# Performance work log

Measured on AMD Instinct MI355X. Metric: run time of the kernel, lower is better.

## Reference

```python
import jax, jax.numpy as jnp
import numpy as np

N_NODES = 50000
N_EDGES = 800000
N_NF = 16
N_EF = 8
HID = 300
MSG = 128
N_HIDDEN = 300
N_PRED = 8
N_GRAPHS = 64


def _lin_init(key, fan_in, fan_out):
    kw, kb = jax.random.split(key)
    lim = 1.0 / np.sqrt(fan_in)
    w = jax.random.uniform(kw, (fan_in, fan_out), minval=-lim, maxval=lim, dtype=jnp.float32)
    b = jax.random.uniform(kb, (fan_out,), minval=-lim, maxval=lim, dtype=jnp.float32)
    return w, b


def setup_inputs() -> dict:
    key = jax.random.key(0)
    ks = jax.random.split(key, 16)
    x = jax.random.normal(ks[0], (N_NODES, N_NF), dtype=jnp.float32)
    edge_index = jax.random.randint(ks[1], (2, N_EDGES), 0, N_NODES, dtype=jnp.int32)
    edge_attr = jax.random.normal(ks[2], (N_EDGES, N_EF), dtype=jnp.float32)
    batch = jnp.sort(jax.random.randint(ks[3], (N_NODES,), 0, N_GRAPHS, dtype=jnp.int32))
    # message MLP: (2*n_nf+n_ef) -> 300 -> 300 -> 300 -> msg_dim
    mw1, mb1 = _lin_init(ks[4], 2 * N_NF + N_EF, HID)
    mw2, mb2 = _lin_init(ks[5], HID, HID)
    mw3, mb3 = _lin_init(ks[6], HID, HID)
    mw4, mb4 = _lin_init(ks[7], HID, MSG)
    # node MLP: msg_dim -> 300 -> 300 -> 300 -> n_hidden
    nw1, nb1 = _lin_init(ks[8], MSG, HID)
    nw2, nb2 = _lin_init(ks[9], HID, HID)
    nw3, nb3 = _lin_init(ks[10], HID, HID)
    nw4, nb4 = _lin_init(ks[11], HID, N_HIDDEN)
    # final linear: n_hidden -> n_predict
    lw, lb = _lin_init(ks[12], N_HIDDEN, N_PRED)
    return {
        "x": x, "edge_index": edge_index, "edge_attr": edge_attr, "batch": batch,
        "mw1": mw1, "mb1": mb1, "mw2": mw2, "mb2": mb2, "mw3": mw3, "mb3": mb3,
        "mw4": mw4, "mb4": mb4,
        "nw1": nw1, "nb1": nb1, "nw2": nw2, "nb2": nb2, "nw3": nw3, "nb3": nb3,
        "nw4": nw4, "nb4": nb4, "lw": lw, "lb": lb,
    }


def reference(x, edge_index, edge_attr, batch,
              mw1, mb1, mw2, mb2, mw3, mb3, mw4, mb4,
              nw1, nb1, nw2, nb2, nw3, nb3, nw4, nb4, lw, lb):
    src = edge_index[0]  # x_j (source, PyG flow source_to_target)
    dst = edge_index[1]  # x_i (target), also scatter destination
    # message: cat([x_i, x_j, e_ij]) -> MLP
    tmp = jnp.concatenate([x[dst], x[src], edge_attr], axis=1)  # [E, 2*n_nf+n_ef]
    h = jax.nn.relu(tmp @ mw1 + mb1)
    h = jax.nn.relu(h @ mw2 + mb2)
    h = jax.nn.relu(h @ mw3 + mb3)
    msg = h @ mw4 + mb4  # [E, msg_dim]
    # aggregate: scatter-add into target nodes
    aggr = jax.ops.segment_sum(msg, dst, num_segments=N_NODES)  # [N, msg_dim]
    # update: node MLP
    h = jax.nn.relu(aggr @ nw1 + nb1)
    h = jax.nn.relu(h @ nw2 + nb2)
    h = jax.nn.relu(h @ nw3 + nb3)
    node = h @ nw4 + nb4  # [N, n_hidden]
    # global mean pool over graphs
    sums = jax.ops.segment_sum(node, batch, num_segments=N_GRAPHS)
    counts = jax.ops.segment_sum(jnp.ones((node.shape[0],), node.dtype), batch, num_segments=N_GRAPHS)
    pooled = sums / jnp.maximum(counts, 1.0)[:, None]  # [G, n_hidden]
    # dropout(p=0.5, training=self.training) is identity in eval mode
    return pooled @ lw + lb  # [G, n_predict]
```

## Files before the change

### kernel.cpp

```cpp
#include <hip/hip_runtime.h>
#include <hip/hip_bf16.h>
#include <stdint.h>

#define E_TOTAL 800000
#define NNODES  50000
#define NGRAPHS 64
#define NPRED   8
#define MPAD    50048
#define EBLK    6250
#define NBLK    391

#define TILE_B  40960
#define SCR_B   81920
#define LDSZ    (2*TILE_B + SCR_B)

typedef short v8s __attribute__((ext_vector_type(8)));
typedef float v4f __attribute__((ext_vector_type(4)));
typedef float f4  __attribute__((ext_vector_type(4)));

__device__ __forceinline__ void gload_lds16(const void* g, void* l) {
    __builtin_amdgcn_global_load_lds(
        (const __attribute__((address_space(1))) uint32_t*)g,
        (__attribute__((address_space(3))) uint32_t*)l, 16, 0, 0);
}

__device__ __forceinline__ short f2bf_s(float f) {
    __hip_bfloat16 h = __float2bfloat16(f);
    return *reinterpret_cast<short*>(&h);
}

template <bool EDGE>
__global__ __launch_bounds__(512)
void chain_kernel(const float* __restrict__ x, const int* __restrict__ ei,
                  const float* __restrict__ ea,
                  const __hip_bfloat16* __restrict__ aggrb,
                  const char* __restrict__ wimg,
                  const float* __restrict__ b1, const float* __restrict__ b2,
                  const float* __restrict__ b3, const float* __restrict__ b4,
                  float* __restrict__ outp)
{
    __shared__ __align__(16) char lds[LDSZ];
    const int tid  = threadIdx.x;
    const int lane = tid & 63;
    const int wave = tid >> 6;
    const int wr   = wave >> 2;
    const int wc   = wave & 3;
    const int l15  = lane & 15;
    const int kk   = lane >> 4;
    char* scr = lds + 2*TILE_B;
    const int rowbase = blockIdx.x*128 + wr*64;

    constexpr int KT1 = EDGE ? 1 : 2;
    constexpr int T   = KT1 + 15;

    auto stagef = [&](int t, int slot_){
        const char* s = wimg + (size_t)t*TILE_B + (size_t)tid*16;
        char* d = lds + slot_*TILE_B + wave*1024;
#pragma unroll
        for (int i = 0; i < 5; ++i) gload_lds16(s + i*8192, d + i*8192);
    };

    v4f acc[4][5];
#pragma unroll
    for (int p = 0; p < 4; ++p)
#pragma unroll
        for (int n = 0; n < 5; ++n) acc[p][n] = (v4f){0.f,0.f,0.f,0.f};

    float bb1[5], bb2[5], bb3[5], bb4[5];
#pragma unroll
    for (int n = 0; n < 5; ++n) {
        int colb = wc*80 + n*16 + l15;
        bb1[n] = b1[colb]; bb2[n] = b2[colb]; bb3[n] = b3[colb];
        if (EDGE) bb4[n] = (n < 2) ? b4[wc*32 + n*16 + l15] : 0.f;
        else      bb4[n] = b4[colb];
    }

    v8s af1[KT1][4][2];
    if (EDGE) {
#pragma unroll
        for (int p = 0; p < 4; ++p) {
            const int e = rowbase + p*16 + l15;
            const int nidx = (kk < 2) ? ei[E_TOTAL + e] : ei[e];
            const float* xs = x + (size_t)nidx*16 + (kk & 1)*8;
            f4 p0 = *(const f4*)xs, p1 = *(const f4*)(xs + 4);
            v8s a0, a1;
#pragma unroll
            for (int j = 0; j < 4; ++j) { a0[j] = f2bf_s(p0[j]); a0[4+j] = f2bf_s(p1[j]); }
            if (kk == 0) {
                const float* es = ea + (size_t)e*8;
                f4 q0 = *(const f4*)es, q1 = *(const f4*)(es + 4);
#pragma unroll
                for (int j = 0; j < 4; ++j) { a1[j] = f2bf_s(q0[j]); a1[4+j] = f2bf_s(q1[j]); }
            } else {
#pragma unroll
                for (int j = 0; j < 8; ++j) a1[j] = 0;
            }
            af1[0][p][0] = a0; af1[0][p][1] = a1;
        }
    } else {
#pragma unroll
        for (int p = 0; p < 4; ++p) {
            const int grow = rowbase + p*16 + l15;
#pragma unroll
            for (int t2 = 0; t2 < KT1; ++t2)
#pragma unroll
                for (int h = 0; h < 2; ++h)
                    af1[t2][p][h] = *(const v8s*)((const char*)aggrb +
                        (size_t)grow*256 + t2*128 + h*64 + kk*16);
        }
    }

    stagef(0, 0);
    int tt = 0, slot = 0;

#define TILE_BEGIN()                                                            \
    { asm volatile("s_waitcnt vmcnt(0)" ::: "memory");                          \
      __builtin_amdgcn_s_barrier();                                             \
      if (tt + 1 < T) stagef(tt + 1, slot ^ 1); }

#define TILE_END()  { ++tt; slot ^= 1; }

#define MFMA_TILE(A_, NT_, CB_)                                                 \
    { const char* sl_ = lds + slot*TILE_B;                                      \
      _Pragma("unroll")                                                         \
      for (int h_ = 0; h_ < 2; ++h_) {                                          \
        _Pragma("unroll")                                                       \
        for (int n_ = 0; n_ < NT_; ++n_) {                                      \
          int r_ = (CB_) + n_*16 + l15;                                         \
          v8s b_ = *(const v8s*)(sl_ + r_*128 + ((((h_<<2)|kk) ^ (r_&7))<<4));  \
          _Pragma("unroll")                                                     \
          for (int p_ = 0; p_ < 4; ++p_)                                        \
            acc[p_][n_] = __builtin_amdgcn_mfma_f32_16x16x32_bf16(              \
                (A_)[p_][h_], b_, acc[p_][n_], 0, 0, 0);                        \
        } } }

#define LOAD_AFRAG(KT_, A_)                                                     \
    { _Pragma("unroll")                                                         \
      for (int p_ = 0; p_ < 4; ++p_)                                            \
        _Pragma("unroll")                                                       \
        for (int h_ = 0; h_ < 2; ++h_) {                                        \
          int c_ = ((KT_)*8 + h_*4 + kk) ^ (l15 & 7);                           \
          (A_)[p_][h_] = *(const v8s*)(scr + (wr*64 + p_*16 + l15)*640 + (c_<<4)); \
        } }

#define DUMP_RELU(BB_)                                                          \
    { __builtin_amdgcn_s_barrier();        \
      _Pragma("unroll")                                                         \
      for (int p_ = 0; p_ < 4; ++p_)                                            \
        _Pragma("unroll")                                                       \
        for (int n_ = 0; n_ < 5; ++n_) {                                        \
          int col_ = wc*80 + n_*16 + l15;                                       \
          _Pragma("unroll")                                                     \
          for (int rr_ = 0; rr_ < 4; ++rr_) {                                   \
            int row_ = wr*64 + p_*16 + kk*4 + rr_;                              \
            float v_ = fmaxf(acc[p_][n_][rr_] + (BB_)[n_], 0.f);                \
            *(__hip_bfloat16*)(scr + row_*640 +                                 \
                (((col_>>3) ^ (row_&7))<<4) + (col_&7)*2) = __float2bfloat16(v_); \
          }                                                                     \
          acc[p_][n_] = (v4f){0.f,0.f,0.f,0.f};                                 \
        }                                                                       \
      asm volatile("s_waitcnt lgkmcnt(0)" ::: "memory"); }

#pragma unroll
    for (int kt = 0; kt < KT1; ++kt) { TILE_BEGIN(); MFMA_TILE(af1[kt], 5, wc*80); TILE_END(); }
    DUMP_RELU(bb1);
#pragma unroll
    for (int kt = 0; kt < 5; ++kt) {
        TILE_BEGIN(); v8s A_[4][2]; LOAD_AFRAG(kt, A_); MFMA_TILE(A_, 5, wc*80); TILE_END();
    }
    DUMP_RELU(bb2);
#pragma unroll
    for (int kt = 0; kt < 5; ++kt) {
        TILE_BEGIN(); v8s A_[4][2]; LOAD_AFRAG(kt, A_); MFMA_TILE(A_, 5, wc*80); TILE_END();
    }
    DUMP_RELU(bb3);
    if (EDGE) {
#pragma unroll
        for (int kt = 0; kt < 5; ++kt) {
            TILE_BEGIN(); v8s A_[4][2]; LOAD_AFRAG(kt, A_); MFMA_TILE(A_, 2, wc*32); TILE_END();
        }
#pragma unroll
        for (int p = 0; p < 4; ++p) {
#pragma unroll
            for (int rr = 0; rr < 4; ++rr) {
                int erow = rowbase + p*16 + kk*4 + rr;
                int d = ei[E_TOTAL + erow];
                float* ag = outp + (size_t)d*128;
#pragma unroll
                for (int n = 0; n < 2; ++n) {
                    int col = wc*32 + n*16 + l15;
                    atomicAdd(ag + col, acc[p][n][rr] + bb4[n]);
                }
            }
        }
    } else {
#pragma unroll
        for (int kt = 0; kt < 5; ++kt) {
            TILE_BEGIN(); v8s A_[4][2]; LOAD_AFRAG(kt, A_); MFMA_TILE(A_, 5, wc*80); TILE_END();
        }
#pragma unroll
        for (int p = 0; p < 4; ++p) {
#pragma unroll
            for (int n = 0; n < 5; ++n) {
                int col = wc*80 + n*16 + l15;
#pragma unroll
                for (int rr = 0; rr < 4; ++rr) {
                    int grow = rowbase + p*16 + kk*4 + rr;
                    outp[(size_t)grow*320 + col] = acc[p][n][rr] + bb4[n];
                }
            }
        }
    }
#undef TILE_BEGIN
#undef TILE_END
#undef MFMA_TILE
#undef LOAD_AFRAG
#undef DUMP_RELU
}

__global__ void repack_tiles(const float* __restrict__ src, char* __restrict__ img,
                             int K, int N, int KT)
{
    int t = blockIdx.x*256 + threadIdx.x;
    if (t >= KT*20480) return;
    int k64  = t & 63;
    int r    = (t >> 6) % 320;
    int tile = t / 20480;
    int kg   = tile*64 + k64;
    float v = (r < N && kg < K) ? src[(size_t)kg*N + r] : 0.f;
    size_t addr = (size_t)tile*TILE_B + (size_t)r*128 +
                  ((((k64>>3) ^ (r&7)))<<4) + (k64&7)*2;
    *(__hip_bfloat16*)(img + addr) = __float2bfloat16(v);
}

__global__ void pad_bias(const float* __restrict__ src, float* __restrict__ dst,
                         int N, int Npad)
{
    int t = blockIdx.x*256 + threadIdx.x;
    if (t < Npad) dst[t] = (t < N) ? src[t] : 0.f;
}

__global__ void cvt_aggr(const float* __restrict__ aggr, __hip_bfloat16* __restrict__ out)
{
    int t = blockIdx.x*256 + threadIdx.x;
    int row = t >> 7;
    float v = (row < NNODES) ? aggr[t] : 0.f;
    out[t] = __float2bfloat16(v);
}

__global__ void graph_starts_kernel(const int* __restrict__ batch,
                                    int* __restrict__ starts)
{
    int g = threadIdx.x;
    if (g > NGRAPHS) return;
    int lo = 0, hi = NNODES;
    while (lo < hi) {
        int mid = (lo + hi) >> 1;
        if (batch[mid] < g) lo = mid + 1; else hi = mid;
    }
    starts[g] = lo;
}

__global__ void pool_kernel(const float* __restrict__ node,
                            const int* __restrict__ starts,
                            float* __restrict__ pooled)
{
    __shared__ float red[8][32];
    int g   = blockIdx.x;
    int col = blockIdx.y*32 + (threadIdx.x & 31);
    int rl  = threadIdx.x >> 5;
    int s = starts[g], e = starts[g + 1];
    float sum = 0.f;
    if (col < 300)
        for (int i = s + rl; i < e; i += 8) sum += node[(size_t)i*320 + col];
    red[rl][threadIdx.x & 31] = sum;
    __syncthreads();
    if (rl == 0 && col < 300) {
        float tot = 0.f;
#pragma unroll
        for (int r = 0; r < 8; ++r) tot += red[r][threadIdx.x & 31];
        float cnt = (float)(e - s);
        pooled[g*300 + col] = tot / fmaxf(cnt, 1.0f);
    }
}

__global__ void final_kernel(const float* __restrict__ pooled,
                             const float* __restrict__ lw,
                             const float* __restrict__ lb,
                             float* __restrict__ out)
{
    int t = threadIdx.x;
    int g = t / NPRED, p = t % NPRED;
    float s = lb[p];
    for (int k = 0; k < 300; ++k)
        s = fmaf(pooled[g*300 + k], lw[k*NPRED + p], s);
    out[g*NPRED + p] = s;
}

extern "C" void kernel_launch(void* const* d_in, const int* in_sizes, int n_in,
                              void* d_out, int out_size, void* d_ws, size_t ws_size,
                              hipStream_t stream)
{
    const float* x     = (const float*)d_in[0];
    const int*   ei    = (const int*)d_in[1];
    const float* ea    = (const float*)d_in[2];
    const int*   batch = (const int*)d_in[3];
    const float* mw[4] = {(const float*)d_in[4], (const float*)d_in[6],
                          (const float*)d_in[8], (const float*)d_in[10]};
    const float* mb[4] = {(const float*)d_in[5], (const float*)d_in[7],
                          (const float*)d_in[9], (const float*)d_in[11]};
    const float* nw[4] = {(const float*)d_in[12], (const float*)d_in[14],
                          (const float*)d_in[16], (const float*)d_in[18]};
    const float* nb[4] = {(const float*)d_in[13], (const float*)d_in[15],
                          (const float*)d_in[17], (const float*)d_in[19]};
    const float* lw = (const float*)d_in[20];
    const float* lb = (const float*)d_in[21];
    float* out = (float*)d_out;

    char* ws = (char*)d_ws;
    size_t off = 0;
    auto alloc = [&](size_t bytes) -> void* {
        void* p = ws + off;
        off += (bytes + 255) & ~(size_t)255;
        return p;
    };

    float*          aggr   = (float*)alloc((size_t)MPAD*128*4);
    __hip_bfloat16* aggrb  = (__hip_bfloat16*)alloc((size_t)MPAD*128*2);
    float*          node   = (float*)alloc((size_t)MPAD*320*4);
    char*           wimg_e = (char*)alloc((size_t)16*TILE_B);
    char*           wimg_n = (char*)alloc((size_t)17*TILE_B);
    float* mbp[4]; float* nbp[4];
    for (int i = 0; i < 4; ++i) { mbp[i] = (float*)alloc(320*4); nbp[i] = (float*)alloc(320*4); }
    float* pooled = (float*)alloc(64*300*4);
    int*   starts = (int*)alloc(65*4);

    const int mK[4]  = {40, 300, 300, 300},  mN[4]  = {300, 300, 300, 128};
    const int nK[4]  = {128, 300, 300, 300}, nN[4]  = {300, 300, 300, 300};
    const int mKT[4] = {1, 5, 5, 5},         nKT[4] = {2, 5, 5, 5};
    {
        size_t te = 0, tn = 0;
        for (int i = 0; i < 4; ++i) {
            repack_tiles<<<mKT[i]*80, 256, 0, stream>>>(mw[i], wimg_e + te*TILE_B,
                                                        mK[i], mN[i], mKT[i]);
            te += mKT[i];
            repack_tiles<<<nKT[i]*80, 256, 0, stream>>>(nw[i], wimg_n + tn*TILE_B,
                                                        nK[i], nN[i], nKT[i]);
            tn += nKT[i];
            pad_bias<<<2, 256, 0, stream>>>(mb[i], mbp[i], mN[i], 320);
            pad_bias<<<2, 256, 0, stream>>>(nb[i], nbp[i], nN[i], 320);
        }
    }
    hipMemsetAsync(aggr, 0, (size_t)NNODES*128*4, stream);
    graph_starts_kernel<<<1, 128, 0, stream>>>(batch, starts);

    chain_kernel<true><<<EBLK, 512, 0, stream>>>(
        x, ei, ea, nullptr, wimg_e, mbp[0], mbp[1], mbp[2], mbp[3], aggr);

    cvt_aggr<<<(MPAD*128)/256, 256, 0, stream>>>(aggr, aggrb);
    chain_kernel<false><<<NBLK, 512, 0, stream>>>(
        x, ei, ea, aggrb, wimg_n, nbp[0], nbp[1], nbp[2], nbp[3], node);

    pool_kernel<<<dim3(64, 10), 256, 0, stream>>>(node, starts, pooled);
    final_kernel<<<1, 512, 0, stream>>>(pooled, lw, lb, out);
}
```

Baseline: 855.9 us.

## Halve block tile and K-tile size to fit two blocks per CU

Blocks shrink from 512 to 256 threads covering 64 rows instead of 128, and weight K-tiles shrink from 64 to 32 columns with a new swizzled packing layout. LDS per block is halved so two blocks can co-reside per CU, aiming to overlap barriers and weight staging across blocks. The cost is twice as many tile iterations and barriers, and each block stages weights for only half as many rows, which doubles weight traffic per row.

```diff
diff --git a/kernel.cpp b/kernel.cpp
--- a/kernel.cpp
+++ b/kernel.cpp
@@ -7,11 +7,11 @@
 #define NGRAPHS 64
 #define NPRED   8
 #define MPAD    50048
-#define EBLK    6250
-#define NBLK    391
-
-#define TILE_B  40960
-#define SCR_B   81920
+#define EBLK    12500
+#define NBLK    782
+
+#define TILE_B  20480
+#define SCR_B   40960
 #define LDSZ    (2*TILE_B + SCR_B)
 
 typedef short v8s __attribute__((ext_vector_type(8)));
@@ -30,7 +30,7 @@
 }
 
 template <bool EDGE>
-__global__ __launch_bounds__(512)
+__global__ __launch_bounds__(256, 2)
 void chain_kernel(const float* __restrict__ x, const int* __restrict__ ei,
                   const float* __restrict__ ea,
                   const __hip_bfloat16* __restrict__ aggrb,
@@ -42,22 +42,20 @@
     __shared__ __align__(16) char lds[LDSZ];
     const int tid  = threadIdx.x;
     const int lane = tid & 63;
-    const int wave = tid >> 6;
-    const int wr   = wave >> 2;
-    const int wc   = wave & 3;
+    const int wc   = tid >> 6;
     const int l15  = lane & 15;
     const int kk   = lane >> 4;
     char* scr = lds + 2*TILE_B;
-    const int rowbase = blockIdx.x*128 + wr*64;
-
-    constexpr int KT1 = EDGE ? 1 : 2;
-    constexpr int T   = KT1 + 15;
+    const int rowbase = blockIdx.x*64;
+
+    constexpr int KT1 = EDGE ? 2 : 4;
+    constexpr int T   = KT1 + 30;
 
     auto stagef = [&](int t, int slot_){
         const char* s = wimg + (size_t)t*TILE_B + (size_t)tid*16;
-        char* d = lds + slot_*TILE_B + wave*1024;
-#pragma unroll
-        for (int i = 0; i < 5; ++i) gload_lds16(s + i*8192, d + i*8192);
+        char* d = lds + slot_*TILE_B + wc*1024;
+#pragma unroll
+        for (int i = 0; i < 5; ++i) gload_lds16(s + i*4096, d + i*4096);
     };
 
     v4f acc[4][5];
@@ -75,7 +73,7 @@
         else      bb4[n] = b4[colb];
     }
 
-    v8s af1[KT1][4][2];
+    v8s af1[KT1][4];
     if (EDGE) {
 #pragma unroll
         for (int p = 0; p < 4; ++p) {
@@ -95,18 +93,16 @@
 #pragma unroll
                 for (int j = 0; j < 8; ++j) a1[j] = 0;
             }
-            af1[0][p][0] = a0; af1[0][p][1] = a1;
+            af1[0][p] = a0; af1[1][p] = a1;
         }
     } else {
 #pragma unroll
         for (int p = 0; p < 4; ++p) {
             const int grow = rowbase + p*16 + l15;
 #pragma unroll
-            for (int t2 = 0; t2 < KT1; ++t2)
-#pragma unroll
-                for (int h = 0; h < 2; ++h)
-                    af1[t2][p][h] = *(const v8s*)((const char*)aggrb +
-                        (size_t)grow*256 + t2*128 + h*64 + kk*16);
+            for (int kt = 0; kt < KT1; ++kt)
+                af1[kt][p] = *(const v8s*)((const char*)aggrb +
+                    (size_t)grow*256 + kt*64 + kk*16);
         }
     }
 
@@ -120,28 +116,25 @@
 
 #define TILE_END()  { ++tt; slot ^= 1; }
 
-#define MFMA_TILE(A_, NT_, CB_)                                                 \
+#define MFMA_TILE(AF_, NT_, CB_)                                                \
     { const char* sl_ = lds + slot*TILE_B;                                      \
       _Pragma("unroll")                                                         \
-      for (int h_ = 0; h_ < 2; ++h_) {                                          \
+      for (int n_ = 0; n_ < NT_; ++n_) {                                        \
+        int r_ = (CB_) + n_*16 + l15;                                           \
+        int ch_ = (kk | ((r_&1)<<2)) ^ ((r_>>1)&7);                             \
+        v8s b_ = *(const v8s*)(sl_ + (r_>>1)*128 + (ch_<<4));                   \
         _Pragma("unroll")                                                       \
-        for (int n_ = 0; n_ < NT_; ++n_) {                                      \
-          int r_ = (CB_) + n_*16 + l15;                                         \
-          v8s b_ = *(const v8s*)(sl_ + r_*128 + ((((h_<<2)|kk) ^ (r_&7))<<4));  \
-          _Pragma("unroll")                                                     \
-          for (int p_ = 0; p_ < 4; ++p_)                                        \
-            acc[p_][n_] = __builtin_amdgcn_mfma_f32_16x16x32_bf16(              \
-                (A_)[p_][h_], b_, acc[p_][n_], 0, 0, 0);                        \
-        } } }
+        for (int p_ = 0; p_ < 4; ++p_)                                          \
+          acc[p_][n_] = __builtin_amdgcn_mfma_f32_16x16x32_bf16(                \
+              (AF_)[p_], b_, acc[p_][n_], 0, 0, 0);                             \
+      } }
 
 #define LOAD_AFRAG(KT_, A_)                                                     \
     { _Pragma("unroll")                                                         \
-      for (int p_ = 0; p_ < 4; ++p_)                                            \
-        _Pragma("unroll")                                                       \
-        for (int h_ = 0; h_ < 2; ++h_) {                                        \
-          int c_ = ((KT_)*8 + h_*4 + kk) ^ (l15 & 7);                           \
-          (A_)[p_][h_] = *(const v8s*)(scr + (wr*64 + p_*16 + l15)*640 + (c_<<4)); \
-        } }
+      for (int p_ = 0; p_ < 4; ++p_) {                                          \
+        int c_ = ((KT_)*4 + kk) ^ (l15 & 7);                                    \
+        (A_)[p_] = *(const v8s*)(scr + (p_*16 + l15)*640 + (c_<<4));            \
+      } }
 
 #define DUMP_RELU(BB_)                                                          \
     { __builtin_amdgcn_s_barrier();        \
@@ -152,7 +145,7 @@
           int col_ = wc*80 + n_*16 + l15;                                       \
           _Pragma("unroll")                                                     \
           for (int rr_ = 0; rr_ < 4; ++rr_) {                                   \
-            int row_ = wr*64 + p_*16 + kk*4 + rr_;                              \
+            int row_ = p_*16 + kk*4 + rr_;                                      \
             float v_ = fmaxf(acc[p_][n_][rr_] + (BB_)[n_], 0.f);                \
             *(__hip_bfloat16*)(scr + row_*640 +                                 \
                 (((col_>>3) ^ (row_&7))<<4) + (col_&7)*2) = __float2bfloat16(v_); \
@@ -165,19 +158,19 @@
     for (int kt = 0; kt < KT1; ++kt) { TILE_BEGIN(); MFMA_TILE(af1[kt], 5, wc*80); TILE_END(); }
     DUMP_RELU(bb1);
 #pragma unroll
-    for (int kt = 0; kt < 5; ++kt) {
-        TILE_BEGIN(); v8s A_[4][2]; LOAD_AFRAG(kt, A_); MFMA_TILE(A_, 5, wc*80); TILE_END();
+    for (int kt = 0; kt < 10; ++kt) {
+        TILE_BEGIN(); v8s A_[4]; LOAD_AFRAG(kt, A_); MFMA_TILE(A_, 5, wc*80); TILE_END();
     }
     DUMP_RELU(bb2);
 #pragma unroll
-    for (int kt = 0; kt < 5; ++kt) {
-        TILE_BEGIN(); v8s A_[4][2]; LOAD_AFRAG(kt, A_); MFMA_TILE(A_, 5, wc*80); TILE_END();
+    for (int kt = 0; kt < 10; ++kt) {
+        TILE_BEGIN(); v8s A_[4]; LOAD_AFRAG(kt, A_); MFMA_TILE(A_, 5, wc*80); TILE_END();
     }
     DUMP_RELU(bb3);
     if (EDGE) {
 #pragma unroll
-        for (int kt = 0; kt < 5; ++kt) {
-            TILE_BEGIN(); v8s A_[4][2]; LOAD_AFRAG(kt, A_); MFMA_TILE(A_, 2, wc*32); TILE_END();
+        for (int kt = 0; kt < 10; ++kt) {
+            TILE_BEGIN(); v8s A_[4]; LOAD_AFRAG(kt, A_); MFMA_TILE(A_, 2, wc*32); TILE_END();
         }
 #pragma unroll
         for (int p = 0; p < 4; ++p) {
@@ -195,8 +188,8 @@
         }
     } else {
 #pragma unroll
-        for (int kt = 0; kt < 5; ++kt) {
-            TILE_BEGIN(); v8s A_[4][2]; LOAD_AFRAG(kt, A_); MFMA_TILE(A_, 5, wc*80); TILE_END();
+        for (int kt = 0; kt < 10; ++kt) {
+            TILE_BEGIN(); v8s A_[4]; LOAD_AFRAG(kt, A_); MFMA_TILE(A_, 5, wc*80); TILE_END();
         }
 #pragma unroll
         for (int p = 0; p < 4; ++p) {
@@ -222,14 +215,17 @@
                              int K, int N, int KT)
 {
     int t = blockIdx.x*256 + threadIdx.x;
-    if (t >= KT*20480) return;
-    int k64  = t & 63;
-    int r    = (t >> 6) % 320;
-    int tile = t / 20480;
-    int kg   = tile*64 + k64;
+    if (t >= KT*10240) return;
+    int tile = t / 10240;
+    int rem  = t - tile*10240;
+    int r    = rem >> 5;
+    int k32  = rem & 31;
+    int c4   = k32 >> 3;
+    int j    = k32 & 7;
+    int kg   = tile*32 + k32;
     float v = (r < N && kg < K) ? src[(size_t)kg*N + r] : 0.f;
-    size_t addr = (size_t)tile*TILE_B + (size_t)r*128 +
-                  ((((k64>>3) ^ (r&7)))<<4) + (k64&7)*2;
+    int ch = (c4 | ((r&1)<<2)) ^ ((r>>1)&7);
+    size_t addr = (size_t)tile*TILE_B + (size_t)(r>>1)*128 + (ch<<4) + j*2;
     *(__hip_bfloat16*)(img + addr) = __float2bfloat16(v);
 }
 
@@ -328,8 +324,8 @@
     float*          aggr   = (float*)alloc((size_t)MPAD*128*4);
     __hip_bfloat16* aggrb  = (__hip_bfloat16*)alloc((size_t)MPAD*128*2);
     float*          node   = (float*)alloc((size_t)MPAD*320*4);
-    char*           wimg_e = (char*)alloc((size_t)16*TILE_B);
-    char*           wimg_n = (char*)alloc((size_t)17*TILE_B);
+    char*           wimg_e = (char*)alloc((size_t)32*TILE_B);
+    char*           wimg_n = (char*)alloc((size_t)34*TILE_B);
     float* mbp[4]; float* nbp[4];
     for (int i = 0; i < 4; ++i) { mbp[i] = (float*)alloc(320*4); nbp[i] = (float*)alloc(320*4); }
     float* pooled = (float*)alloc(64*300*4);
@@ -337,14 +333,14 @@
 
     const int mK[4]  = {40, 300, 300, 300},  mN[4]  = {300, 300, 300, 128};
     const int nK[4]  = {128, 300, 300, 300}, nN[4]  = {300, 300, 300, 300};
-    const int mKT[4] = {1, 5, 5, 5},         nKT[4] = {2, 5, 5, 5};
+    const int mKT[4] = {2, 10, 10, 10},      nKT[4] = {4, 10, 10, 10};
     {
         size_t te = 0, tn = 0;
         for (int i = 0; i < 4; ++i) {
-            repack_tiles<<<mKT[i]*80, 256, 0, stream>>>(mw[i], wimg_e + te*TILE_B,
+            repack_tiles<<<mKT[i]*40, 256, 0, stream>>>(mw[i], wimg_e + te*TILE_B,
                                                         mK[i], mN[i], mKT[i]);
             te += mKT[i];
-            repack_tiles<<<nKT[i]*80, 256, 0, stream>>>(nw[i], wimg_n + tn*TILE_B,
+            repack_tiles<<<nKT[i]*40, 256, 0, stream>>>(nw[i], wimg_n + tn*TILE_B,
                                                         nK[i], nN[i], nKT[i]);
             tn += nKT[i];
             pad_bias<<<2, 256, 0, stream>>>(mb[i], mbp[i], mN[i], 320);
@@ -354,11 +350,11 @@
     hipMemsetAsync(aggr, 0, (size_t)NNODES*128*4, stream);
     graph_starts_kernel<<<1, 128, 0, stream>>>(batch, starts);
 
-    chain_kernel<true><<<EBLK, 512, 0, stream>>>(
+    chain_kernel<true><<<EBLK, 256, 0, stream>>>(
         x, ei, ea, nullptr, wimg_e, mbp[0], mbp[1], mbp[2], mbp[3], aggr);
 
     cvt_aggr<<<(MPAD*128)/256, 256, 0, stream>>>(aggr, aggrb);
-    chain_kernel<false><<<NBLK, 512, 0, stream>>>(
+    chain_kernel<false><<<NBLK, 256, 0, stream>>>(
         x, ei, ea, aggrb, wimg_n, nbp[0], nbp[1], nbp[2], nbp[3], node);
 
     pool_kernel<<<dim3(64, 10), 256, 0, stream>>>(node, starts, pooled);
```

Result: no change. 872.7 us (+2.0%).
